# Performance work log

Measured on AMD Instinct MI355X. Metric: run time of the kernel, lower is better.

## Reference

```python
import jax, jax.numpy as jnp
import numpy as np

D_MODEL = 1024
N_HEADS = 16
D_K = D_MODEL // N_HEADS


def setup_inputs() -> dict:
    key = jax.random.key(0)
    ks = jax.random.split(key, 9)
    B, S = 2, 2048
    scale = 1.0 / np.sqrt(D_MODEL)
    inp = {
        "X": jax.random.normal(ks[0], (B, S, D_MODEL), dtype=jnp.float32),
        "Wq": jax.random.normal(ks[1], (D_MODEL, D_MODEL), dtype=jnp.float32) * scale,
        "bq": jnp.zeros((D_MODEL,), dtype=jnp.float32),
        "Wk": jax.random.normal(ks[2], (D_MODEL, D_MODEL), dtype=jnp.float32) * scale,
        "bk": jnp.zeros((D_MODEL,), dtype=jnp.float32),
        "Wv": jax.random.normal(ks[3], (D_MODEL, D_MODEL), dtype=jnp.float32) * scale,
        "bv": jnp.zeros((D_MODEL,), dtype=jnp.float32),
        "Wo": jax.random.normal(ks[4], (D_MODEL, D_MODEL), dtype=jnp.float32) * scale,
        "bo": jnp.zeros((D_MODEL,), dtype=jnp.float32),
    }
    return inp


def reference(X, Wq, bq, Wk, bk, Wv, bv, Wo, bo):
    B, S, _ = X.shape
    # QKV projections (torch Linear: x @ W.T + b; here W stored as [in, out])
    Q = X @ Wq + bq
    K = X @ Wk + bk
    V = X @ Wv + bv
    # [B, S, H, Dk] -> [B, H, S, Dk]
    def split_heads(t):
        return t.reshape(B, S, N_HEADS, D_K).transpose(0, 2, 1, 3)
    Q, K, V = split_heads(Q), split_heads(K), split_heads(V)
    scores = jnp.einsum('bhqd,bhkd->bhqk', Q, K) / jnp.sqrt(jnp.float32(D_K))
    attn = jax.nn.softmax(scores, axis=-1)
    out = jnp.einsum('bhqk,bhkd->bhqd', attn, V)  # [B, H, S, Dk]
    out = out.transpose(0, 2, 1, 3).reshape(B, S, D_MODEL)
    return out @ Wo + bo
```

## Files before the change

### kernel.cpp

```cpp
#include <hip/hip_runtime.h>
#include <hip/hip_bf16.h>


typedef __attribute__((ext_vector_type(8))) short short8;
typedef __attribute__((ext_vector_type(4))) float f32x4;
typedef unsigned short u16;
typedef unsigned int u32;

static __device__ __forceinline__ u16 f2bf(float f) {
    union { float f; u32 u; } c; c.f = f;
    u32 u = c.u;
    u32 r = u + 0x7fffu + ((u >> 16) & 1u);
    return (u16)(r >> 16);
}
static __device__ __forceinline__ float bf2f(u16 x) {
    union { u32 u; float f; } c; c.u = ((u32)x) << 16;
    return c.f;
}

#define GL1(p) ((const __attribute__((address_space(1))) void*)(p))
#define LD3(p) ((__attribute__((address_space(3))) void*)(p))
static __device__ __forceinline__ void gld16(const void* g, void* l) {
    __builtin_amdgcn_global_load_lds(GL1(g), LD3(l), 16, 0, 0);
}

#define Q_PRESCALE 0.18033688011112042f

__global__ __launch_bounds__(256) void convert_x(const float* __restrict__ X,
                                                 u16* __restrict__ Xb) {
    int i = (blockIdx.x * 256 + threadIdx.x) * 4;
    float4 v = *reinterpret_cast<const float4*>(X + i);
    ushort4 o;
    o.x = f2bf(v.x); o.y = f2bf(v.y); o.z = f2bf(v.z); o.w = f2bf(v.w);
    *reinterpret_cast<ushort4*>(Xb + i) = o;
}

__global__ __launch_bounds__(256) void transpose_w(
    const float* __restrict__ W0, const float* __restrict__ W1,
    const float* __restrict__ W2, const float* __restrict__ W3,
    u16* __restrict__ T0, u16* __restrict__ T1,
    u16* __restrict__ T2, u16* __restrict__ T3)
{
    const float* W; u16* T;
    switch (blockIdx.z) {
        case 0: W = W0; T = T0; break;
        case 1: W = W1; T = T1; break;
        case 2: W = W2; T = T2; break;
        default: W = W3; T = T3; break;
    }
    __shared__ float tile[64][65];
    int t = threadIdx.x;
    int k0 = blockIdx.y * 64, n0 = blockIdx.x * 64;
    int r = t / 16, c4 = (t % 16) * 4;
    #pragma unroll
    for (int p = 0; p < 4; p++) {
        int row = p * 16 + r;
        float4 v = *reinterpret_cast<const float4*>(W + (k0 + row) * 1024 + n0 + c4);
        tile[row][c4 + 0] = v.x; tile[row][c4 + 1] = v.y;
        tile[row][c4 + 2] = v.z; tile[row][c4 + 3] = v.w;
    }
    __syncthreads();
    #pragma unroll
    for (int p = 0; p < 4; p++) {
        int nrow = p * 16 + r;
        ushort4 o;
        o.x = f2bf(tile[c4 + 0][nrow]); o.y = f2bf(tile[c4 + 1][nrow]);
        o.z = f2bf(tile[c4 + 2][nrow]); o.w = f2bf(tile[c4 + 3][nrow]);
        *reinterpret_cast<ushort4*>(T + (n0 + nrow) * 1024 + k0 + c4) = o;
    }
}

__global__ __launch_bounds__(256) void gemm_qkv(
    const u16* __restrict__ Xb,
    const u16* __restrict__ Wtq, const u16* __restrict__ Wtk, const u16* __restrict__ Wtv,
    const float* __restrict__ bq, const float* __restrict__ bk, const float* __restrict__ bv,
    u16* __restrict__ Qb, u16* __restrict__ Kb, u16* __restrict__ Vb)
{
    const u16* Wt; const float* bias; u16* dst; float osc;
    if (blockIdx.z == 0)      { Wt = Wtq; bias = bq; dst = Qb; osc = Q_PRESCALE; }
    else if (blockIdx.z == 1) { Wt = Wtk; bias = bk; dst = Kb; osc = 1.0f; }
    else                      { Wt = Wtv; bias = bv; dst = Vb; osc = 1.0f; }

    __shared__ __align__(16) u16 As[128 * 32];
    __shared__ __align__(16) u16 Bs[128 * 32];
    int t = threadIdx.x;
    int w = t >> 6, lane = t & 63, l15 = lane & 15, quad = lane >> 4;
    int wm = (w >> 1) * 64, wn = (w & 1) * 64;
    int row0 = blockIdx.y * 128, col0 = blockIdx.x * 128;

    int drow = lane >> 2;
    int gc8 = (((lane & 3) ^ (drow & 3))) * 8;

    int asw = ((quad ^ (l15 & 3)) & 3) * 8;

    f32x4 acc[4][4];
    #pragma unroll
    for (int i = 0; i < 4; i++)
        #pragma unroll
        for (int j = 0; j < 4; j++)
            acc[i][j] = (f32x4){0.f, 0.f, 0.f, 0.f};

    for (int k0 = 0; k0 < 1024; k0 += 32) {
        __syncthreads();
        #pragma unroll
        for (int q = 0; q < 2; q++) {
            int rr = w * 32 + q * 16;
            gld16(&Xb[(row0 + rr + drow) * 1024 + k0 + gc8], &As[rr * 32]);
            gld16(&Wt[(col0 + rr + drow) * 1024 + k0 + gc8], &Bs[rr * 32]);
        }
        __syncthreads();
        short8 a[4], b[4];
        #pragma unroll
        for (int i = 0; i < 4; i++)
            a[i] = *reinterpret_cast<const short8*>(&As[(wm + i * 16 + l15) * 32 + asw]);
        #pragma unroll
        for (int j = 0; j < 4; j++)
            b[j] = *reinterpret_cast<const short8*>(&Bs[(wn + j * 16 + l15) * 32 + asw]);
        #pragma unroll
        for (int i = 0; i < 4; i++)
            #pragma unroll
            for (int j = 0; j < 4; j++)
                acc[i][j] = __builtin_amdgcn_mfma_f32_16x16x32_bf16(a[i], b[j], acc[i][j], 0, 0, 0);
    }
    #pragma unroll
    for (int i = 0; i < 4; i++) {
        int rowb = row0 + wm + i * 16 + quad * 4;
        #pragma unroll
        for (int j = 0; j < 4; j++) {
            int col = col0 + wn + j * 16 + l15;
            float bb = bias[col];
            int h = col >> 6, d = col & 63;
            #pragma unroll
            for (int r = 0; r < 4; r++) {
                int gr = rowb + r;
                int b_ = gr >> 11, s = gr & 2047;
                dst[(((b_ << 4) + h) * 2048 + s) * 64 + d] = f2bf((acc[i][j][r] + bb) * osc);
            }
        }
    }
}

__global__ __launch_bounds__(256) void transpose_v(const u16* __restrict__ Vb,
                                                   u16* __restrict__ Vtg) {
    int bh = blockIdx.y;
    int s0 = blockIdx.x * 64;
    __shared__ u16 tile[64][72];
    int t = threadIdx.x;
    const u16* src = Vb + bh * (2048 * 64);
    u16* dst = Vtg + bh * (64 * 2048);
    int sl = t >> 3, d8 = (t & 7) * 8;
    #pragma unroll
    for (int p = 0; p < 2; p++) {
        int row = p * 32 + sl;
        *reinterpret_cast<uint4*>(&tile[row][d8]) =
            *reinterpret_cast<const uint4*>(&src[(s0 + row) * 64 + d8]);
    }
    __syncthreads();
    #pragma unroll
    for (int p = 0; p < 2; p++) {
        int dr = p * 32 + sl;
        union { u16 s[8]; uint4 v; } pk;
        #pragma unroll
        for (int i = 0; i < 8; i++) pk.s[i] = tile[d8 + i][dr];
        *reinterpret_cast<uint4*>(&dst[dr * 2048 + s0 + d8]) = pk.v;
    }
}

__global__ __launch_bounds__(256) void attn(
    const u16* __restrict__ Qb, const u16* __restrict__ Kb,
    const u16* __restrict__ Vtg, u16* __restrict__ Opart, float* __restrict__ Lsum)
{
    int qt = blockIdx.x, bh = blockIdx.y, sp = blockIdx.z;
    int b_ = bh >> 4, h = bh & 15;
    const u16* Qp = Qb + bh * (2048 * 64);
    const u16* Kp = Kb + bh * (2048 * 64);
    const u16* Vp = Vtg + bh * (64 * 2048);
    u16* Op = Opart + sp * (4096 * 1024);
    float* Lp = Lsum + sp * (32 * 2048) + bh * 2048;

    __shared__ __align__(16) u16 Ks[64 * 64];
    __shared__ __align__(16) u16 Vt[64 * 64];
    __shared__ __align__(16) u16 Ps[128 * 64];

    int t = threadIdx.x, w = t >> 6, lane = t & 63, l15 = lane & 15, quad = lane >> 4;

    short8 qf[2][2];
    #pragma unroll
    for (int f = 0; f < 2; f++)
        #pragma unroll
        for (int ds = 0; ds < 2; ds++)
            qf[f][ds] = *reinterpret_cast<const short8*>(
                &Qp[(qt * 128 + w * 32 + f * 16 + l15) * 64 + ds * 32 + quad * 8]);

    int di = lane >> 3;
    int dc8 = ((lane & 7) ^ di) * 8;

    int rl = l15 & 7, rh = l15 >> 3;
    int koff[4][2];
    #pragma unroll
    for (int j = 0; j < 4; j++)
        #pragma unroll
        for (int ds = 0; ds < 2; ds++)
            koff[j][ds] = (j * 2 + rh) * 512 + rl * 64 + (((ds * 4 + quad) ^ rl) & 7) * 8;

    int pw[2][4];
    #pragma unroll
    for (int f = 0; f < 2; f++)
        #pragma unroll
        for (int j = 0; j < 4; j++)
            pw[f][j] = (w * 32 + f * 16 + quad * 4) * 64 + ((16 * j + l15 - 16 * quad) & 63);
    int s4 = (l15 >> 2) & 3;
    int pr[2][2];
    #pragma unroll
    for (int f = 0; f < 2; f++)
        #pragma unroll
        for (int ks = 0; ks < 2; ks++)
            pr[f][ks] = (w * 32 + f * 16 + l15) * 64 + ((ks * 32 + quad * 8 - 16 * s4) & 63);

    f32x4 acc[2][4];
    f32x4 lsum[2];
    #pragma unroll
    for (int f = 0; f < 2; f++) {
        lsum[f] = (f32x4){0.f, 0.f, 0.f, 0.f};
        #pragma unroll
        for (int j = 0; j < 4; j++) acc[f][j] = (f32x4){0.f, 0.f, 0.f, 0.f};
    }

    for (int kt = 0; kt < 16; kt++) {
        int kbase = sp * 1024 + kt * 64;
        __syncthreads();
        #pragma unroll
        for (int sg = 0; sg < 2; sg++) {
            int seg = w * 2 + sg;
            gld16(&Kp[(kbase + seg * 8 + di) * 64 + dc8], &Ks[seg * 512]);
            gld16(&Vp[(seg * 8 + di) * 2048 + kbase + dc8], &Vt[seg * 512]);
        }
        __syncthreads();

        f32x4 sc[2][4];
        #pragma unroll
        for (int j = 0; j < 4; j++) {
            f32x4 s0 = (f32x4){0.f, 0.f, 0.f, 0.f};
            f32x4 s1 = (f32x4){0.f, 0.f, 0.f, 0.f};
            #pragma unroll
            for (int ds = 0; ds < 2; ds++) {
                short8 kf = *reinterpret_cast<const short8*>(&Ks[koff[j][ds]]);
                s0 = __builtin_amdgcn_mfma_f32_16x16x32_bf16(qf[0][ds], kf, s0, 0, 0, 0);
                s1 = __builtin_amdgcn_mfma_f32_16x16x32_bf16(qf[1][ds], kf, s1, 0, 0, 0);
            }
            sc[0][j] = s0; sc[1][j] = s1;
        }

        #pragma unroll
        for (int f = 0; f < 2; f++)
            #pragma unroll
            for (int j = 0; j < 4; j++)
                #pragma unroll
                for (int r = 0; r < 4; r++) {
                    float p = __builtin_amdgcn_exp2f(sc[f][j][r]);
                    lsum[f][r] += p;
                    union { float fv; u32 uv; } c; c.fv = p;
                    Ps[pw[f][j] + r * 64] = (u16)((c.uv + 0x8000u) >> 16);
                }

        #pragma unroll
        for (int ks = 0; ks < 2; ks++) {
            short8 pf0 = *reinterpret_cast<const short8*>(&Ps[pr[0][ks]]);
            short8 pf1 = *reinterpret_cast<const short8*>(&Ps[pr[1][ks]]);
            #pragma unroll
            for (int j = 0; j < 4; j++) {
                short8 vf = *reinterpret_cast<const short8*>(&Vt[koff[j][ks]]);
                acc[0][j] = __builtin_amdgcn_mfma_f32_16x16x32_bf16(pf0, vf, acc[0][j], 0, 0, 0);
                acc[1][j] = __builtin_amdgcn_mfma_f32_16x16x32_bf16(pf1, vf, acc[1][j], 0, 0, 0);
            }
        }
    }

    #pragma unroll
    for (int f = 0; f < 2; f++)
        #pragma unroll
        for (int r = 0; r < 4; r++) {
            float s = lsum[f][r];
            s += __shfl_xor(s, 1);
            s += __shfl_xor(s, 2);
            s += __shfl_xor(s, 4);
            s += __shfl_xor(s, 8);
            lsum[f][r] = s;
        }
    if (l15 == 0) {
        #pragma unroll
        for (int f = 0; f < 2; f++)
            #pragma unroll
            for (int r = 0; r < 4; r++)
                Lp[qt * 128 + w * 32 + f * 16 + quad * 4 + r] = lsum[f][r];
    }

    #pragma unroll
    for (int f = 0; f < 2; f++)
        #pragma unroll
        for (int j = 0; j < 4; j++)
            #pragma unroll
            for (int r = 0; r < 4; r++) {
                int srow = qt * 128 + w * 32 + f * 16 + quad * 4 + r;
                Op[(b_ * 2048 + srow) * 1024 + h * 64 + j * 16 + l15] = f2bf(acc[f][j][r]);
            }
}

__global__ __launch_bounds__(256) void combine(
    const u16* __restrict__ O0, const u16* __restrict__ O1,
    const float* __restrict__ L0, const float* __restrict__ L1,
    u16* __restrict__ Ob)
{
    int idx8 = (blockIdx.x * 256 + threadIdx.x) * 8;
    int row = idx8 >> 10, col = idx8 & 1023;
    int b_ = row >> 11, s = row & 2047, h = col >> 6;
    int li = (b_ * 16 + h) * 2048 + s;
    float inv = 1.0f / (L0[li] + L1[li]);
    union { uint4 v; u16 s[8]; } ua, ub, uo;
    ua.v = *reinterpret_cast<const uint4*>(&O0[idx8]);
    ub.v = *reinterpret_cast<const uint4*>(&O1[idx8]);
    #pragma unroll
    for (int i = 0; i < 8; i++)
        uo.s[i] = f2bf((bf2f(ua.s[i]) + bf2f(ub.s[i])) * inv);
    *reinterpret_cast<uint4*>(&Ob[idx8]) = uo.v;
}

__global__ __launch_bounds__(256) void gemm_out(
    const u16* __restrict__ Ob, const u16* __restrict__ Wto,
    const float* __restrict__ bo, float* __restrict__ out)
{
    __shared__ __align__(16) u16 As[128 * 32];
    __shared__ __align__(16) u16 Bs[128 * 32];
    int t = threadIdx.x;
    int w = t >> 6, lane = t & 63, l15 = lane & 15, quad = lane >> 4;
    int wm = (w >> 1) * 64, wn = (w & 1) * 64;
    int row0 = blockIdx.y * 128, col0 = blockIdx.x * 128;

    int drow = lane >> 2;
    int gc8 = (((lane & 3) ^ (drow & 3))) * 8;
    int asw = ((quad ^ (l15 & 3)) & 3) * 8;

    f32x4 acc[4][4];
    #pragma unroll
    for (int i = 0; i < 4; i++)
        #pragma unroll
        for (int j = 0; j < 4; j++)
            acc[i][j] = (f32x4){0.f, 0.f, 0.f, 0.f};

    for (int k0 = 0; k0 < 1024; k0 += 32) {
        __syncthreads();
        #pragma unroll
        for (int q = 0; q < 2; q++) {
            int rr = w * 32 + q * 16;
            gld16(&Ob[(row0 + rr + drow) * 1024 + k0 + gc8], &As[rr * 32]);
            gld16(&Wto[(col0 + rr + drow) * 1024 + k0 + gc8], &Bs[rr * 32]);
        }
        __syncthreads();
        short8 a[4], b[4];
        #pragma unroll
        for (int i = 0; i < 4; i++)
            a[i] = *reinterpret_cast<const short8*>(&As[(wm + i * 16 + l15) * 32 + asw]);
        #pragma unroll
        for (int j = 0; j < 4; j++)
            b[j] = *reinterpret_cast<const short8*>(&Bs[(wn + j * 16 + l15) * 32 + asw]);
        #pragma unroll
        for (int i = 0; i < 4; i++)
            #pragma unroll
            for (int j = 0; j < 4; j++)
                acc[i][j] = __builtin_amdgcn_mfma_f32_16x16x32_bf16(a[i], b[j], acc[i][j], 0, 0, 0);
    }
    #pragma unroll
    for (int i = 0; i < 4; i++) {
        int rowb = row0 + wm + i * 16 + quad * 4;
        #pragma unroll
        for (int j = 0; j < 4; j++) {
            int col = col0 + wn + j * 16 + l15;
            float bb = bo[col];
            #pragma unroll
            for (int r = 0; r < 4; r++)
                out[(rowb + r) * 1024 + col] = acc[i][j][r] + bb;
        }
    }
}

extern "C" void kernel_launch(void* const* d_in, const int* in_sizes, int n_in,
                              void* d_out, int out_size, void* d_ws, size_t ws_size,
                              hipStream_t stream) {
    const float* X  = (const float*)d_in[0];
    const float* Wq = (const float*)d_in[1];
    const float* bq = (const float*)d_in[2];
    const float* Wk = (const float*)d_in[3];
    const float* bk = (const float*)d_in[4];
    const float* Wv = (const float*)d_in[5];
    const float* bv = (const float*)d_in[6];
    const float* Wo = (const float*)d_in[7];
    const float* bo = (const float*)d_in[8];
    float* out = (float*)d_out;

    char* ws = (char*)d_ws;
    u16* Xb   = (u16*)(ws);
    u16* Wtq  = (u16*)(ws + (8u  << 20));
    u16* Wtk  = (u16*)(ws + (10u << 20));
    u16* Wtv  = (u16*)(ws + (12u << 20));
    u16* Wto  = (u16*)(ws + (14u << 20));
    u16* Qb   = (u16*)(ws + (16u << 20));
    u16* Kb   = (u16*)(ws + (24u << 20));
    u16* Vb   = (u16*)(ws + (32u << 20));
    u16* Vtg  = (u16*)(ws + (40u << 20));
    u16* Op   = (u16*)(ws + (48u << 20));
    float* Ls = (float*)(ws + (64u << 20));
    u16* Ob   = (u16*)(ws + (65u << 20));

    convert_x  <<<4096, 256, 0, stream>>>(X, Xb);
    transpose_w<<<dim3(16, 16, 4), 256, 0, stream>>>(Wq, Wk, Wv, Wo, Wtq, Wtk, Wtv, Wto);
    gemm_qkv   <<<dim3(8, 32, 3), 256, 0, stream>>>(Xb, Wtq, Wtk, Wtv, bq, bk, bv, Qb, Kb, Vb);
    transpose_v<<<dim3(32, 32), 256, 0, stream>>>(Vb, Vtg);
    attn       <<<dim3(16, 32, 2), 256, 0, stream>>>(Qb, Kb, Vtg, Op, Ls);
    combine    <<<2048, 256, 0, stream>>>(Op, Op + (4096 * 1024), Ls, Ls + (32 * 2048), Ob);
    gemm_out   <<<dim3(8, 32), 256, 0, stream>>>(Ob, Wto, bo, out);
}
```

Measured before the change: 228.5 us.

## Transpose score MFMA, pack P stores, and strengthen LDS swizzles

The attention kernel now computes scores as K·Q^T so each lane holds four consecutive keys for one query row. That lets P be written to LDS as packed 8-byte stores with an XOR swizzle instead of 16 scalar u16 stores, and row sums become one scalar per lane reduced across quads with two shuffles. The GEMM kernels' LDS swizzle adds a second XOR term to cut bank conflicts on fragment reads. This changes the LDS layouts and index maps, so a mismatch between the write and read swizzles would silently corrupt results.

```diff
diff --git a/kernel.cpp b/kernel.cpp
--- a/kernel.cpp
+++ b/kernel.cpp
@@ -89,9 +89,9 @@
     int row0 = blockIdx.y * 128, col0 = blockIdx.x * 128;
 
     int drow = lane >> 2;
-    int gc8 = (((lane & 3) ^ (drow & 3))) * 8;
-
-    int asw = ((quad ^ (l15 & 3)) & 3) * 8;
+    int gc8 = ((lane & 3) ^ (drow & 3) ^ ((drow >> 2) & 3)) * 8;
+
+    int asw = ((quad ^ (l15 & 3) ^ ((l15 >> 2) & 3)) & 3) * 8;
 
     f32x4 acc[4][4];
     #pragma unroll
@@ -203,28 +203,26 @@
         for (int ds = 0; ds < 2; ds++)
             koff[j][ds] = (j * 2 + rh) * 512 + rl * 64 + (((ds * 4 + quad) ^ rl) & 7) * 8;
 
-    int pw[2][4];
+    int pwt[2][4];
     #pragma unroll
     for (int f = 0; f < 2; f++)
         #pragma unroll
         for (int j = 0; j < 4; j++)
-            pw[f][j] = (w * 32 + f * 16 + quad * 4) * 64 + ((16 * j + l15 - 16 * quad) & 63);
-    int s4 = (l15 >> 2) & 3;
-    int pr[2][2];
+            pwt[f][j] = (w * 32 + f * 16 + l15) * 64 +
+                        (((2 * j + (quad >> 1)) ^ rl) * 8) + (quad & 1) * 4;
+    int prt[2][2];
     #pragma unroll
     for (int f = 0; f < 2; f++)
         #pragma unroll
         for (int ks = 0; ks < 2; ks++)
-            pr[f][ks] = (w * 32 + f * 16 + l15) * 64 + ((ks * 32 + quad * 8 - 16 * s4) & 63);
+            prt[f][ks] = (w * 32 + f * 16 + l15) * 64 + (((4 * ks + quad) ^ rl) * 8);
 
     f32x4 acc[2][4];
-    f32x4 lsum[2];
-    #pragma unroll
-    for (int f = 0; f < 2; f++) {
-        lsum[f] = (f32x4){0.f, 0.f, 0.f, 0.f};
+    float lsum[2] = {0.f, 0.f};
+    #pragma unroll
+    for (int f = 0; f < 2; f++)
         #pragma unroll
         for (int j = 0; j < 4; j++) acc[f][j] = (f32x4){0.f, 0.f, 0.f, 0.f};
-    }
 
     for (int kt = 0; kt < 16; kt++) {
         int kbase = sp * 1024 + kt * 64;
@@ -245,8 +243,8 @@
             #pragma unroll
             for (int ds = 0; ds < 2; ds++) {
                 short8 kf = *reinterpret_cast<const short8*>(&Ks[koff[j][ds]]);
-                s0 = __builtin_amdgcn_mfma_f32_16x16x32_bf16(qf[0][ds], kf, s0, 0, 0, 0);
-                s1 = __builtin_amdgcn_mfma_f32_16x16x32_bf16(qf[1][ds], kf, s1, 0, 0, 0);
+                s0 = __builtin_amdgcn_mfma_f32_16x16x32_bf16(kf, qf[0][ds], s0, 0, 0, 0);
+                s1 = __builtin_amdgcn_mfma_f32_16x16x32_bf16(kf, qf[1][ds], s1, 0, 0, 0);
             }
             sc[0][j] = s0; sc[1][j] = s1;
         }
@@ -254,19 +252,24 @@
         #pragma unroll
         for (int f = 0; f < 2; f++)
             #pragma unroll
-            for (int j = 0; j < 4; j++)
-                #pragma unroll
-                for (int r = 0; r < 4; r++) {
-                    float p = __builtin_amdgcn_exp2f(sc[f][j][r]);
-                    lsum[f][r] += p;
-                    union { float fv; u32 uv; } c; c.fv = p;
-                    Ps[pw[f][j] + r * 64] = (u16)((c.uv + 0x8000u) >> 16);
-                }
+            for (int j = 0; j < 4; j++) {
+                float p0 = __builtin_amdgcn_exp2f(sc[f][j][0]);
+                float p1 = __builtin_amdgcn_exp2f(sc[f][j][1]);
+                float p2 = __builtin_amdgcn_exp2f(sc[f][j][2]);
+                float p3 = __builtin_amdgcn_exp2f(sc[f][j][3]);
+                lsum[f] += (p0 + p1) + (p2 + p3);
+                union { float fv; u32 uv; } c0, c1, c2, c3;
+                c0.fv = p0; c1.fv = p1; c2.fv = p2; c3.fv = p3;
+                uint2 pk;
+                pk.x = ((c0.uv + 0x8000u) >> 16) | ((c1.uv + 0x8000u) & 0xffff0000u);
+                pk.y = ((c2.uv + 0x8000u) >> 16) | ((c3.uv + 0x8000u) & 0xffff0000u);
+                *reinterpret_cast<uint2*>(&Ps[pwt[f][j]]) = pk;
+            }
 
         #pragma unroll
         for (int ks = 0; ks < 2; ks++) {
-            short8 pf0 = *reinterpret_cast<const short8*>(&Ps[pr[0][ks]]);
-            short8 pf1 = *reinterpret_cast<const short8*>(&Ps[pr[1][ks]]);
+            short8 pf0 = *reinterpret_cast<const short8*>(&Ps[prt[0][ks]]);
+            short8 pf1 = *reinterpret_cast<const short8*>(&Ps[prt[1][ks]]);
             #pragma unroll
             for (int j = 0; j < 4; j++) {
                 short8 vf = *reinterpret_cast<const short8*>(&Vt[koff[j][ks]]);
@@ -277,22 +280,16 @@
     }
 
     #pragma unroll
-    for (int f = 0; f < 2; f++)
-        #pragma unroll
-        for (int r = 0; r < 4; r++) {
-            float s = lsum[f][r];
-            s += __shfl_xor(s, 1);
-            s += __shfl_xor(s, 2);
-            s += __shfl_xor(s, 4);
-            s += __shfl_xor(s, 8);
-            lsum[f][r] = s;
-        }
-    if (l15 == 0) {
+    for (int f = 0; f < 2; f++) {
+        float s = lsum[f];
+        s += __shfl_xor(s, 16);
+        s += __shfl_xor(s, 32);
+        lsum[f] = s;
+    }
+    if (quad == 0) {
         #pragma unroll
         for (int f = 0; f < 2; f++)
-            #pragma unroll
-            for (int r = 0; r < 4; r++)
-                Lp[qt * 128 + w * 32 + f * 16 + quad * 4 + r] = lsum[f][r];
+            Lp[qt * 128 + w * 32 + f * 16 + l15] = lsum[f];
     }
 
     #pragma unroll
@@ -337,8 +334,8 @@
     int row0 = blockIdx.y * 128, col0 = blockIdx.x * 128;
 
     int drow = lane >> 2;
-    int gc8 = (((lane & 3) ^ (drow & 3))) * 8;
-    int asw = ((quad ^ (l15 & 3)) & 3) * 8;
+    int gc8 = ((lane & 3) ^ (drow & 3) ^ ((drow >> 2) & 3)) * 8;
+    int asw = ((quad ^ (l15 & 3) ^ ((l15 >> 2) & 3)) & 3) * 8;
 
     f32x4 acc[4][4];
     #pragma unroll
```

Measured after the change: 225.8 us. Within noise of the previous version (-1.2%).
